# Kernel tuning notes

Hardware: AMD Instinct MI355X
Metric: run time of the kernel (lower is better)

Reference implementation:

```python
import jax, jax.numpy as jnp
import numpy as np

N_VAR = 524288   # code.n
DV = 3           # regular variable-node degree
DC = 6           # regular check-node degree
N_CHK = N_VAR * DV // DC
T = 10           # max_iterations


def setup_inputs() -> dict:
    key = jax.random.key(0)
    k1, k2, k3 = jax.random.split(key, 3)
    rng = np.random.default_rng(0)
    # Regular (3,6) Tanner graph via random socket permutation (edge list == H sparsity)
    edge_var = np.repeat(np.arange(N_VAR, dtype=np.int32), DV)
    edge_chk = rng.permutation(np.repeat(np.arange(N_CHK, dtype=np.int32), DC)).astype(np.int32)
    llr = jax.random.normal(k1, (N_VAR,), jnp.float32) * 2.0
    beta = jax.random.normal(k2, (T,), jnp.float32) * 0.1   # per-iteration dc-shared offsets
    alpha = jax.random.normal(k3, (T,), jnp.float32) * 0.1  # per-iteration dv-shared offsets
    return {"llr": llr, "beta": beta, "alpha": alpha,
            "edge_var": jnp.asarray(edge_var), "edge_chk": jnp.asarray(edge_chk),
            "n_checks": N_CHK}


def reference(llr, beta, alpha, edge_var, edge_chk, n_checks):
    E = edge_var.shape[0]
    n = llr.shape[0]
    e_idx = jnp.arange(E)

    def step(carry, ba):
        v2c, _ = carry
        b, a = ba
        mags = jnp.abs(v2c)
        sgn = jnp.sign(v2c)
        # per-check min / argmin(first) / second-min over incoming edge magnitudes
        min1 = jax.ops.segment_min(mags, edge_chk, num_segments=n_checks)
        amin = jax.ops.segment_min(jnp.where(mags == min1[edge_chk], e_idx, E),
                                   edge_chk, num_segments=n_checks)
        is_amin = e_idx == amin[edge_chk]
        min2 = jax.ops.segment_min(jnp.where(is_amin, jnp.inf, mags),
                                   edge_chk, num_segments=n_checks)
        min2 = jnp.where(jnp.isinf(min2), min1, min2)  # degree-1 checks: min2 = min1
        raw = jnp.where(is_amin, min2[edge_chk], min1[edge_chk])
        # product of signs excluding self (signs are +-1)
        sprod = jax.ops.segment_prod(sgn, edge_chk, num_segments=n_checks)
        c2v = sprod[edge_chk] * sgn * (jax.nn.relu(raw - b) - a)
        # variable node: extrinsic sum
        tot = jax.ops.segment_sum(c2v, edge_var, num_segments=n)
        v2c_new = llr[edge_var] + tot[edge_var] - c2v
        return (v2c_new, c2v), None

    v2c0 = llr[edge_var]
    (v2c_f, c2v_f), _ = jax.lax.scan(step, (v2c0, jnp.zeros_like(v2c0)), (beta, alpha))
    posterior = llr + jax.ops.segment_sum(c2v_f, edge_var, num_segments=n)
    decoded_bits = (posterior < 0).astype(jnp.int32)
    return decoded_bits, posterior
```

## Files before the change

### kernel.cpp

```cpp
#include <hip/hip_runtime.h>
#include <math.h>

#define DC_C 6
#define NRANGE 8
#define BCH 2048

__global__ void build_a(const int* __restrict__ edge_chk,
                        const float* __restrict__ llr,
                        int* __restrict__ cnt,
                        int* __restrict__ pos,
                        float* __restrict__ v2c_e,
                        int E) {
    int e = blockIdx.x * blockDim.x + threadIdx.x;
    if (e >= E) return;
    int c = edge_chk[e];
    int j = atomicAdd(&cnt[c], 1);
    pos[e] = c * DC_C + j;
    v2c_e[e] = llr[e / 3];
}

__global__ void build_b(const int* __restrict__ pos,
                        int* __restrict__ idx,
                        int E) {
    int r = blockIdx.x & (NRANGE - 1);
    int chunk = blockIdx.x >> 3;
    int lo = r * (E / NRANGE);
    int hi = lo + (E / NRANGE);
    int base = chunk * BCH;
    for (int k = threadIdx.x; k < BCH; k += 256) {
        int e = base + k;
        if (e >= E) break;
        int s = pos[e];
        if (s >= lo && s < hi) idx[s] = e;
    }
}

__global__ void check_kernel(const float* __restrict__ v2c_e,
                             const int* __restrict__ idx,
                             float* __restrict__ c2v_s,
                             const float* __restrict__ beta,
                             const float* __restrict__ alpha,
                             int t, int n_chk) {
    int c = blockIdx.x * blockDim.x + threadIdx.x;
    if (c >= n_chk) return;
    float b = beta[t];
    float a = alpha[t];
    int base = c * DC_C;
    int e[DC_C];
#pragma unroll
    for (int j = 0; j < DC_C; ++j) e[j] = idx[base + j];
    float sg[DC_C], mg[DC_C];
    float sprod = 1.0f;
    float m1 = INFINITY, m2 = INFINITY;
#pragma unroll
    for (int j = 0; j < DC_C; ++j) {
        float v = v2c_e[e[j]];
        float s = (v > 0.0f) ? 1.0f : ((v < 0.0f) ? -1.0f : 0.0f);
        float m = fabsf(v);
        sg[j] = s;
        mg[j] = m;
        sprod *= s;
        if (m < m1) { m2 = m1; m1 = m; }
        else if (m < m2) { m2 = m; }
    }
#pragma unroll
    for (int j = 0; j < DC_C; ++j) {
        float raw = (mg[j] == m1) ? m2 : m1;
        float val = fmaxf(raw - b, 0.0f) - a;
        c2v_s[base + j] = sprod * sg[j] * val;
    }
}

__global__ void var_kernel(const float* __restrict__ c2v_s,
                           const int* __restrict__ pos,
                           const float* __restrict__ llr,
                           float* __restrict__ v2c_e,
                           int n) {
    int v = blockIdx.x * blockDim.x + threadIdx.x;
    if (v >= n) return;
    int p0 = pos[v * 3 + 0];
    int p1 = pos[v * 3 + 1];
    int p2 = pos[v * 3 + 2];
    float c0 = c2v_s[p0];
    float c1 = c2v_s[p1];
    float c2 = c2v_s[p2];
    float tot = (c0 + c1) + c2;
    float t = llr[v] + tot;
    v2c_e[v * 3 + 0] = t - c0;
    v2c_e[v * 3 + 1] = t - c1;
    v2c_e[v * 3 + 2] = t - c2;
}

__global__ void final_kernel(const float* __restrict__ c2v_s,
                             const int* __restrict__ pos,
                             const float* __restrict__ llr,
                             float* __restrict__ out,
                             int n) {
    int v = blockIdx.x * blockDim.x + threadIdx.x;
    if (v >= n) return;
    int p0 = pos[v * 3 + 0];
    int p1 = pos[v * 3 + 1];
    int p2 = pos[v * 3 + 2];
    float c0 = c2v_s[p0];
    float c1 = c2v_s[p1];
    float c2 = c2v_s[p2];
    float post = llr[v] + ((c0 + c1) + c2);
    out[v] = (post < 0.0f) ? 1.0f : 0.0f;
    out[n + v] = post;
}

extern "C" void kernel_launch(void* const* d_in, const int* in_sizes, int n_in,
                              void* d_out, int out_size, void* d_ws, size_t ws_size,
                              hipStream_t stream) {
    const float* llr      = (const float*)d_in[0];
    const float* beta     = (const float*)d_in[1];
    const float* alpha    = (const float*)d_in[2];
    const int*   edge_chk = (const int*)d_in[4];

    const int n  = in_sizes[0];
    const int T  = in_sizes[1];
    const int E  = in_sizes[3];
    const int n_chk = E / DC_C;

    char* ws = (char*)d_ws;
    int*   cnt   = (int*)ws;
    int*   pos   = (int*)(ws + (size_t)n_chk * 4);
    int*   idx   = pos + E;
    float* v2c_e = (float*)(idx + E);
    float* c2v_s = v2c_e + E;

    hipMemsetAsync(cnt, 0, (size_t)n_chk * 4, stream);
    build_a<<<(E + 255) / 256, 256, 0, stream>>>(edge_chk, llr, cnt, pos, v2c_e, E);
    {
        int chunks = (E + BCH - 1) / BCH;
        build_b<<<chunks * NRANGE, 256, 0, stream>>>(pos, idx, E);
    }
    for (int t = 0; t < T; ++t) {
        check_kernel<<<(n_chk + 255) / 256, 256, 0, stream>>>(v2c_e, idx, c2v_s,
                                                              beta, alpha, t, n_chk);
        if (t + 1 < T) {
            var_kernel<<<(n + 255) / 256, 256, 0, stream>>>(c2v_s, pos, llr, v2c_e, n);
        } else {
            final_kernel<<<(n + 255) / 256, 256, 0, stream>>>(c2v_s, pos, llr,
                                                              (float*)d_out, n);
        }
    }
}
```

Measured before the change: 438.7 us.

## Vectorize build kernels, read llr directly in first check, shrink blocks

build_a and build_b now process four edges per thread using int4 loads and stores. The initial v2c copy is removed: the first check iteration gathers llr[e/3] directly. check_kernel loads indices and stores outputs as float2. All iteration kernels move to 128-thread blocks with launch bounds. Together these aim to cut memory traffic and instruction overhead in setup and the per-iteration gathers, but they assume E is divisible by 4 and that the index arrays are suitably aligned.

```diff
diff --git a/kernel.cpp b/kernel.cpp
--- a/kernel.cpp
+++ b/kernel.cpp
@@ -5,78 +5,100 @@
 #define NRANGE 8
 #define BCH 2048
 
-__global__ void build_a(const int* __restrict__ edge_chk,
-                        const float* __restrict__ llr,
-                        int* __restrict__ cnt,
-                        int* __restrict__ pos,
-                        float* __restrict__ v2c_e,
-                        int E) {
-    int e = blockIdx.x * blockDim.x + threadIdx.x;
-    if (e >= E) return;
-    int c = edge_chk[e];
-    int j = atomicAdd(&cnt[c], 1);
-    pos[e] = c * DC_C + j;
-    v2c_e[e] = llr[e / 3];
+__global__ __launch_bounds__(256) void build_a(const int4* __restrict__ edge_chk4,
+                                               int* __restrict__ cnt,
+                                               int4* __restrict__ pos4,
+                                               int E4) {
+    int t = blockIdx.x * blockDim.x + threadIdx.x;
+    if (t >= E4) return;
+    int4 c = edge_chk4[t];
+    int j0 = atomicAdd(&cnt[c.x], 1);
+    int j1 = atomicAdd(&cnt[c.y], 1);
+    int j2 = atomicAdd(&cnt[c.z], 1);
+    int j3 = atomicAdd(&cnt[c.w], 1);
+    pos4[t] = make_int4(c.x * DC_C + j0, c.y * DC_C + j1,
+                        c.z * DC_C + j2, c.w * DC_C + j3);
 }
 
-__global__ void build_b(const int* __restrict__ pos,
-                        int* __restrict__ idx,
-                        int E) {
+__global__ __launch_bounds__(256) void build_b(const int4* __restrict__ pos4,
+                                               int* __restrict__ idx,
+                                               int E) {
     int r = blockIdx.x & (NRANGE - 1);
     int chunk = blockIdx.x >> 3;
     int lo = r * (E / NRANGE);
     int hi = lo + (E / NRANGE);
-    int base = chunk * BCH;
-    for (int k = threadIdx.x; k < BCH; k += 256) {
-        int e = base + k;
-        if (e >= E) break;
-        int s = pos[e];
-        if (s >= lo && s < hi) idx[s] = e;
+    int base4 = chunk * (BCH / 4);
+    int lim4 = E / 4;
+#pragma unroll
+    for (int rr = 0; rr < 2; ++rr) {
+        int t4 = base4 + rr * 256 + threadIdx.x;
+        if (t4 >= lim4) break;
+        int4 p = pos4[t4];
+        int e = t4 * 4;
+        if (p.x >= lo && p.x < hi) idx[p.x] = e;
+        if (p.y >= lo && p.y < hi) idx[p.y] = e + 1;
+        if (p.z >= lo && p.z < hi) idx[p.z] = e + 2;
+        if (p.w >= lo && p.w < hi) idx[p.w] = e + 3;
     }
 }
 
-__global__ void check_kernel(const float* __restrict__ v2c_e,
-                             const int* __restrict__ idx,
-                             float* __restrict__ c2v_s,
-                             const float* __restrict__ beta,
-                             const float* __restrict__ alpha,
-                             int t, int n_chk) {
-    int c = blockIdx.x * blockDim.x + threadIdx.x;
+__global__ __launch_bounds__(128, 8) void check_kernel(
+        const float* __restrict__ src,
+        const int* __restrict__ idx,
+        float* __restrict__ c2v_s,
+        const float* __restrict__ beta,
+        const float* __restrict__ alpha,
+        int t, int n_chk, int first) {
+    int c = blockIdx.x * 128 + threadIdx.x;
     if (c >= n_chk) return;
+    int base = c * DC_C;
+    int2 i01 = *(const int2*)(idx + base);
+    int2 i23 = *(const int2*)(idx + base + 2);
+    int2 i45 = *(const int2*)(idx + base + 4);
+    int e[DC_C] = {i01.x, i01.y, i23.x, i23.y, i45.x, i45.y};
+    float v[DC_C];
+    if (first) {
+#pragma unroll
+        for (int j = 0; j < DC_C; ++j) v[j] = src[e[j] / 3];
+    } else {
+#pragma unroll
+        for (int j = 0; j < DC_C; ++j) v[j] = src[e[j]];
+    }
     float b = beta[t];
     float a = alpha[t];
-    int base = c * DC_C;
-    int e[DC_C];
-#pragma unroll
-    for (int j = 0; j < DC_C; ++j) e[j] = idx[base + j];
     float sg[DC_C], mg[DC_C];
     float sprod = 1.0f;
     float m1 = INFINITY, m2 = INFINITY;
 #pragma unroll
     for (int j = 0; j < DC_C; ++j) {
-        float v = v2c_e[e[j]];
-        float s = (v > 0.0f) ? 1.0f : ((v < 0.0f) ? -1.0f : 0.0f);
-        float m = fabsf(v);
+        float x = v[j];
+        float s = (x > 0.0f) ? 1.0f : ((x < 0.0f) ? -1.0f : 0.0f);
+        float m = fabsf(x);
         sg[j] = s;
         mg[j] = m;
         sprod *= s;
         if (m < m1) { m2 = m1; m1 = m; }
         else if (m < m2) { m2 = m; }
     }
+    float o[DC_C];
 #pragma unroll
     for (int j = 0; j < DC_C; ++j) {
         float raw = (mg[j] == m1) ? m2 : m1;
         float val = fmaxf(raw - b, 0.0f) - a;
-        c2v_s[base + j] = sprod * sg[j] * val;
+        o[j] = sprod * sg[j] * val;
     }
+    *(float2*)(c2v_s + base)     = make_float2(o[0], o[1]);
+    *(float2*)(c2v_s + base + 2) = make_float2(o[2], o[3]);
+    *(float2*)(c2v_s + base + 4) = make_float2(o[4], o[5]);
 }
 
-__global__ void var_kernel(const float* __restrict__ c2v_s,
-                           const int* __restrict__ pos,
-                           const float* __restrict__ llr,
-                           float* __restrict__ v2c_e,
-                           int n) {
-    int v = blockIdx.x * blockDim.x + threadIdx.x;
+__global__ __launch_bounds__(128, 8) void var_kernel(
+        const float* __restrict__ c2v_s,
+        const int* __restrict__ pos,
+        const float* __restrict__ llr,
+        float* __restrict__ v2c_e,
+        int n) {
+    int v = blockIdx.x * 128 + threadIdx.x;
     if (v >= n) return;
     int p0 = pos[v * 3 + 0];
     int p1 = pos[v * 3 + 1];
@@ -91,12 +113,13 @@
     v2c_e[v * 3 + 2] = t - c2;
 }
 
-__global__ void final_kernel(const float* __restrict__ c2v_s,
-                             const int* __restrict__ pos,
-                             const float* __restrict__ llr,
-                             float* __restrict__ out,
-                             int n) {
-    int v = blockIdx.x * blockDim.x + threadIdx.x;
+__global__ __launch_bounds__(128, 8) void final_kernel(
+        const float* __restrict__ c2v_s,
+        const int* __restrict__ pos,
+        const float* __restrict__ llr,
+        float* __restrict__ out,
+        int n) {
+    int v = blockIdx.x * 128 + threadIdx.x;
     if (v >= n) return;
     int p0 = pos[v * 3 + 0];
     int p1 = pos[v * 3 + 1];
@@ -130,18 +153,24 @@
     float* c2v_s = v2c_e + E;
 
     hipMemsetAsync(cnt, 0, (size_t)n_chk * 4, stream);
-    build_a<<<(E + 255) / 256, 256, 0, stream>>>(edge_chk, llr, cnt, pos, v2c_e, E);
+    {
+        int E4 = E / 4;
+        build_a<<<(E4 + 255) / 256, 256, 0, stream>>>((const int4*)edge_chk,
+                                                      cnt, (int4*)pos, E4);
+    }
     {
         int chunks = (E + BCH - 1) / BCH;
-        build_b<<<chunks * NRANGE, 256, 0, stream>>>(pos, idx, E);
+        build_b<<<chunks * NRANGE, 256, 0, stream>>>((const int4*)pos, idx, E);
     }
     for (int t = 0; t < T; ++t) {
-        check_kernel<<<(n_chk + 255) / 256, 256, 0, stream>>>(v2c_e, idx, c2v_s,
-                                                              beta, alpha, t, n_chk);
+        const float* src = (t == 0) ? llr : v2c_e;
+        check_kernel<<<(n_chk + 127) / 128, 128, 0, stream>>>(
+            src, idx, c2v_s, beta, alpha, t, n_chk, (t == 0) ? 1 : 0);
         if (t + 1 < T) {
-            var_kernel<<<(n + 255) / 256, 256, 0, stream>>>(c2v_s, pos, llr, v2c_e, n);
+            var_kernel<<<(n + 127) / 128, 128, 0, stream>>>(c2v_s, pos, llr,
+                                                            v2c_e, n);
         } else {
-            final_kernel<<<(n + 255) / 256, 256, 0, stream>>>(c2v_s, pos, llr,
+            final_kernel<<<(n + 127) / 128, 128, 0, stream>>>(c2v_s, pos, llr,
                                                               (float*)d_out, n);
         }
     }
```

Measured after the change: 451.0 us. +2.8%, slower.
